# Performance work log

Measured on AMD Instinct MI355X. Metric: run time of the kernel, lower is better.

The kernel has to match this reference:

```python
import jax, jax.numpy as jnp
import numpy as np

D_MODEL = 256; N_HEADS = 8; N_LEVELS = 4; N_POINTS = 4
D_HEAD = D_MODEL // N_HEADS


def setup_inputs() -> dict:
    key = jax.random.key(0)
    ks = jax.random.split(key, 8)
    N, Lq = 4, 4096
    shapes = np.array([4096, 2048, 1024, 512], dtype=np.int32)  # temporal lengths per level
    Len_in = int(shapes.sum())  # 7680
    start = np.concatenate([[0], np.cumsum(shapes)[:-1]]).astype(np.int32)
    HLP = N_HEADS * N_LEVELS * N_POINTS
    return {
        "query": jax.random.normal(ks[0], (N, Lq, D_MODEL), jnp.float32),
        "reference_points": jax.random.uniform(ks[1], (N, Lq, N_LEVELS, 1), jnp.float32),
        "input_flatten": jax.random.normal(ks[2], (N, Len_in, D_MODEL), jnp.float32),
        "input_spatial_shapes": jnp.asarray(shapes),
        "input_level_start_index": jnp.asarray(start),
        "W_off": jax.random.normal(ks[3], (D_MODEL, HLP), jnp.float32) * 0.01,
        "b_off": jax.random.normal(ks[4], (HLP,), jnp.float32) * 2.0,
        "W_aw": jax.random.normal(ks[5], (D_MODEL, HLP), jnp.float32) * 0.02,
        "b_aw": jnp.zeros((HLP,), jnp.float32),
        "W_v": jax.random.normal(ks[6], (D_MODEL, D_MODEL), jnp.float32) / np.sqrt(D_MODEL).astype(np.float32),
        "b_v": jnp.zeros((D_MODEL,), jnp.float32),
        "W_out": jax.random.normal(ks[7], (D_MODEL, D_MODEL), jnp.float32) / np.sqrt(D_MODEL).astype(np.float32),
        "b_out": jnp.zeros((D_MODEL,), jnp.float32),
    }


def reference(query, reference_points, input_flatten, input_spatial_shapes,
              input_level_start_index, W_off, b_off, W_aw, b_aw, W_v, b_v,
              W_out, b_out):
    N, Lq, C = query.shape
    M, L, P, Dh = N_HEADS, N_LEVELS, N_POINTS, D_HEAD
    S = input_flatten.shape[1]

    value = (input_flatten @ W_v + b_v).reshape(N, S, M, Dh)
    off = (query @ W_off + b_off).reshape(N, Lq, M, L, P)
    aw = jax.nn.softmax((query @ W_aw + b_aw).reshape(N, Lq, M, L * P), axis=-1)
    aw = aw.reshape(N, Lq, M, L, P)

    # reference_points last dim == 1 branch: loc = ref + off / T_l, in [0,1]
    T = input_spatial_shapes.astype(jnp.float32)[None, None, None, :, None]  # [1,1,1,L,1]
    loc = reference_points[:, :, None, :, None, 0] + off / T  # [N,Lq,M,L,P]

    # grid_sample(align_corners=False, padding_mode='border') along W with H=1, y=0.5:
    # pixel coord x = loc*T - 0.5, clamped to [0, T-1], then linear interp.
    x = jnp.clip(loc * T - 0.5, 0.0, T - 1.0)
    x0 = jnp.floor(x)
    w1 = x - x0                                   # frac weight for right neighbor
    i0 = x0.astype(jnp.int32)
    i1 = jnp.minimum(i0 + 1, input_spatial_shapes[None, None, None, :, None] - 1)
    base = input_level_start_index[None, None, None, :, None]
    g0 = i0 + base                                # global flattened indices [N,Lq,M,L,P]
    g1 = i1 + base

    v = value.transpose(0, 2, 1, 3)               # [N,M,S,Dh]

    def gather(idx):
        idxt = idx.transpose(0, 2, 1, 3, 4).reshape(N, M, Lq * L * P, 1)
        return jnp.take_along_axis(v, idxt, axis=2).reshape(N, M, Lq, L, P, Dh)

    s0 = gather(g0)
    s1 = gather(g1)
    w1t = w1.transpose(0, 2, 1, 3, 4)[..., None]   # [N,M,Lq,L,P,1]
    samp = s0 * (1.0 - w1t) + s1 * w1t             # [N,M,Lq,L,P,Dh]

    awt = aw.transpose(0, 2, 1, 3, 4)[..., None]
    out = (samp * awt).sum(axis=(3, 4))            # [N,M,Lq,Dh]
    out = out.transpose(0, 2, 1, 3).reshape(N, Lq, M * Dh)
    return out @ W_out + b_out
```

## Files before the change

### kernel.cpp

```cpp
#include <hip/hip_runtime.h>
#include <hip/hip_bf16.h>
#include <cstddef>
#include <cstdint>

#define D_MODEL   256
#define N_HEADS   8
#define N_LEVELS  4
#define N_POINTS  4
#define D_HEAD    32
#define HLP       128
#define NBATCH    4
#define LQ        4096
#define S_LEN     7680
#define QB        8

typedef __attribute__((ext_vector_type(8))) short  short8;
typedef __attribute__((ext_vector_type(4))) float  f32x4;
typedef __attribute__((ext_vector_type(8))) unsigned short ushort8;

__device__ __forceinline__ unsigned short f2bf(float x) {
    __hip_bfloat16 h = __float2bfloat16(x);
    return *reinterpret_cast<unsigned short*>(&h);
}
__device__ __forceinline__ float bf2f(unsigned short u) {
    unsigned int v = ((unsigned int)u) << 16;
    return *reinterpret_cast<float*>(&v);
}

__device__ __forceinline__ void gload_lds16(const void* g, void* l) {
    __builtin_amdgcn_global_load_lds(
        (const __attribute__((address_space(1))) void*)g,
        (__attribute__((address_space(3))) void*)l,
        16, 0, 0);
}

__global__ __launch_bounds__(256) void prep_kernel(
    const float* __restrict__ W_v,  const float* __restrict__ W_off,
    const float* __restrict__ W_aw, const float* __restrict__ W_out,
    const float* __restrict__ b_off, const float* __restrict__ b_aw,
    unsigned short* __restrict__ Wv_t, unsigned short* __restrict__ Wcat_t,
    unsigned short* __restrict__ Wout_t, float* __restrict__ bcat)
{
    __shared__ float t[64][65];
    const int z   = blockIdx.z;
    const int k0  = blockIdx.y * 64;
    const int n0  = blockIdx.x * 64;
    const int tid = threadIdx.x;

    const float* src; int srcN; int cs; unsigned short* dst;
    if (z == 0)      { src = W_v;   srcN = 256; cs = n0;       dst = Wv_t;  }
    else if (z == 2) { src = W_out; srcN = 256; cs = n0;       dst = Wout_t;}
    else if (n0 < 128){ src = W_off; srcN = 128; cs = n0;      dst = Wcat_t;}
    else             { src = W_aw;  srcN = 128; cs = n0 - 128; dst = Wcat_t;}

    #pragma unroll
    for (int i = 0; i < 16; ++i) {
        int idx = tid + i * 256;
        int kk = idx >> 6, nn = idx & 63;
        t[kk][nn] = src[(size_t)(k0 + kk) * srcN + cs + nn];
    }
    __syncthreads();
    #pragma unroll
    for (int i = 0; i < 16; ++i) {
        int idx = tid + i * 256;
        int nn = idx >> 6, kk = idx & 63;
        dst[(size_t)(n0 + nn) * 256 + k0 + kk] = f2bf(t[kk][nn]);
    }
    if (z == 1 && blockIdx.x == 0 && blockIdx.y == 0) {
        bcat[tid] = (tid < 128) ? b_off[tid] : b_aw[tid - 128];
    }
}

__global__ __launch_bounds__(256) void gemm_vp_kernel(
    const float* __restrict__ inflat, const float* __restrict__ query,
    const unsigned short* __restrict__ Wv_t, const unsigned short* __restrict__ Wcat_t,
    const float* __restrict__ b_v, const float* __restrict__ bcat,
    unsigned short* __restrict__ value3, float* __restrict__ P)
{
    __shared__ alignas(16) unsigned short Abuf[2][4][64][8];
    __shared__ alignas(16) unsigned short Bbuf[2][8][64][8];

    const int job = blockIdx.x;
    const bool is_val = (job < 960);
    const int jj   = is_val ? job : (job - 960);
    const int row0 = (jj >> 1) * 64;
    const int col0 = (jj & 1) * 128;
    const float* A = is_val ? inflat : query;
    const unsigned short* Bt = is_val ? Wv_t : Wcat_t;
    const float* bias = is_val ? b_v : bcat;

    const int tid  = threadIdx.x;
    const int lane = tid & 63;
    const int w    = tid >> 6;
    const int lr   = lane & 15;
    const int lk   = (lane >> 4) * 8;

    const int ar = tid >> 2;
    const int ak = (tid & 3) * 8;
    const int afrag = ar >> 4;
    const int alane = ((ak >> 3) << 4) | (ar & 15);
    const float* Arow = A + (size_t)(row0 + ar) * 256 + ak;
    const unsigned short* Bcol = Bt + (size_t)(col0 + lr) * 256 + lk;

    f32x4 acc[8] = {};

    float4 pa0 = *(const float4*)(Arow);
    float4 pa1 = *(const float4*)(Arow + 4);
    #pragma unroll
    for (int c = 0; c < 2; ++c) {
        const int in = w * 2 + c;
        gload_lds16(Bcol + (size_t)in * 16 * 256, &Bbuf[0][in][0][0]);
    }

    for (int kt = 0; kt < 8; ++kt) {
        const int cur = kt & 1;
        short8 pk;
        pk[0] = (short)f2bf(pa0.x); pk[1] = (short)f2bf(pa0.y);
        pk[2] = (short)f2bf(pa0.z); pk[3] = (short)f2bf(pa0.w);
        pk[4] = (short)f2bf(pa1.x); pk[5] = (short)f2bf(pa1.y);
        pk[6] = (short)f2bf(pa1.z); pk[7] = (short)f2bf(pa1.w);
        *(short8*)&Abuf[cur][afrag][alane][0] = pk;
        __syncthreads();

        if (kt < 7) {
            const int k1 = (kt + 1) * 32;
            pa0 = *(const float4*)(Arow + k1);
            pa1 = *(const float4*)(Arow + k1 + 4);
            #pragma unroll
            for (int c = 0; c < 2; ++c) {
                const int in = w * 2 + c;
                gload_lds16(Bcol + (size_t)in * 16 * 256 + k1, &Bbuf[1 - cur][in][0][0]);
            }
        }

        const short8 af = *(const short8*)&Abuf[cur][w][lane][0];
        #pragma unroll
        for (int j = 0; j < 8; ++j) {
            const short8 bf = *(const short8*)&Bbuf[cur][j][lane][0];
            acc[j] = __builtin_amdgcn_mfma_f32_16x16x32_bf16(af, bf, acc[j], 0, 0, 0);
        }
    }

    const int prow = (lane >> 4) * 4;
    const int pcol = lane & 15;
    const int rbase = row0 + w * 16 + prow;
    if (is_val) {
        const int n  = row0 / S_LEN;
        const int s0 = row0 - n * S_LEN + w * 16 + prow;
        #pragma unroll
        for (int j = 0; j < 8; ++j) {
            const int col = col0 + j * 16 + pcol;
            const float bs = bias[col];
            const int m = col >> 5, d = col & 31;
            unsigned short* dst = value3 + ((size_t)(n * 8 + m) * S_LEN + s0) * 32 + d;
            #pragma unroll
            for (int r = 0; r < 4; ++r)
                dst[(size_t)r * 32] = f2bf(acc[j][r] + bs);
        }
    } else {
        #pragma unroll
        for (int j = 0; j < 8; ++j) {
            const int col = col0 + j * 16 + pcol;
            const float bs = bias[col];
            #pragma unroll
            for (int r = 0; r < 4; ++r)
                P[(size_t)(rbase + r) * 256 + col] = acc[j][r] + bs;
        }
    }
}

__global__ __launch_bounds__(256) void sample_kernel(
    const float* __restrict__ P, const float* __restrict__ refp,
    const int* __restrict__ shapes, const int* __restrict__ lstart,
    const unsigned short* __restrict__ value3,
    unsigned short* __restrict__ tout)
{
    __shared__ int   sG0[QB][130];
    __shared__ float sW [QB][130];
    __shared__ float sA [QB][130];
    __shared__ int   glim[4];

    const int b    = blockIdx.x;
    const int xcd  = b & 7;
    const int n    = xcd >> 1;
    const int half = xcd & 1;
    const int slot = b >> 3;
    const int q0   = (slot * 2 + half) * QB;
    const int nq0  = n * LQ + q0;
    const int tid  = threadIdx.x;

    if (tid < 4) glim[tid] = lstart[tid] + shapes[tid] - 1;

    #pragma unroll
    for (int it = 0; it < 4; ++it) {
        const int idx = tid + it * 256;
        const int q   = idx >> 7;
        const int j   = idx & 127;
        const int l   = (j >> 2) & 3;
        const int nq  = nq0 + q;
        const float off   = __builtin_nontemporal_load(P + (size_t)nq * 256 + j);
        const float logit = __builtin_nontemporal_load(P + (size_t)nq * 256 + 128 + j);
        const float ref   = __builtin_nontemporal_load(refp + (size_t)nq * N_LEVELS + l);
        const int   sh    = shapes[l];
        const float Tf    = (float)sh;
        float x = ref * Tf + off - 0.5f;
        x = fminf(fmaxf(x, 0.0f), Tf - 1.0f);
        const float x0 = floorf(x);
        sG0[q][j] = (int)x0 + lstart[l];
        sW [q][j] = x - x0;
        sA [q][j] = logit;
    }
    __syncthreads();

    const int q  = tid >> 5;
    const int r  = tid & 31;
    const int m  = r >> 2;
    const int ql = r & 3;
    const unsigned short* vb =
        value3 + (size_t)(n * 8 + m) * S_LEN * 32 + ql * 8;

    float e[16];
    float mx = -1e30f;
    #pragma unroll
    for (int i = 0; i < 16; ++i) { e[i] = sA[q][m * 16 + i]; mx = fmaxf(mx, e[i]); }
    float s = 0.f;
    #pragma unroll
    for (int i = 0; i < 16; ++i) { e[i] = __expf(e[i] - mx); s += e[i]; }
    const float rs = 1.0f / s;

    float acc[8] = {};
    #pragma unroll
    for (int i = 0; i < 16; ++i) {
        const int j = m * 16 + i;
        const float a  = e[i] * rs;
        const float ww = sW[q][j];
        const int g0 = sG0[q][j];
        const int g1 = min(g0 + 1, glim[i >> 2]);
        const ushort8 u0 = *(const ushort8*)(vb + (size_t)g0 * 32);
        const ushort8 u1 = *(const ushort8*)(vb + (size_t)g1 * 32);
        #pragma unroll
        for (int d = 0; d < 8; ++d) {
            const float v0 = bf2f(u0[d]);
            const float v1 = bf2f(u1[d]);
            acc[d] += a * (v0 + ww * (v1 - v0));
        }
    }
    ushort8 o;
    #pragma unroll
    for (int d = 0; d < 8; ++d) o[d] = f2bf(acc[d]);
    __builtin_nontemporal_store(o,
        (ushort8*)(tout + (size_t)(nq0 + q) * 256 + m * 32 + ql * 8));
}

__global__ __launch_bounds__(256) void gemm_out_kernel(
    const unsigned short* __restrict__ A,
    const unsigned short* __restrict__ Bt,
    const float* __restrict__ bias,
    float* __restrict__ Cout)
{
    __shared__ alignas(16) unsigned short Abuf[2][4][64][8];
    __shared__ alignas(16) unsigned short Bbuf[2][8][64][8];

    const int jj   = blockIdx.x;
    const int row0 = (jj >> 1) * 64;
    const int col0 = (jj & 1) * 128;

    const int tid  = threadIdx.x;
    const int lane = tid & 63;
    const int w    = tid >> 6;
    const int lr   = lane & 15;
    const int lk   = (lane >> 4) * 8;

    const unsigned short* Arow = A + (size_t)(row0 + w * 16 + lr) * 256 + lk;
    const unsigned short* Bcol = Bt + (size_t)(col0 + lr) * 256 + lk;

    f32x4 acc[8] = {};

    gload_lds16(Arow, &Abuf[0][w][0][0]);
    #pragma unroll
    for (int c = 0; c < 2; ++c) {
        const int in = w * 2 + c;
        gload_lds16(Bcol + (size_t)in * 16 * 256, &Bbuf[0][in][0][0]);
    }

    for (int kt = 0; kt < 8; ++kt) {
        const int cur = kt & 1;
        __syncthreads();

        if (kt < 7) {
            const int k1 = (kt + 1) * 32;
            gload_lds16(Arow + k1, &Abuf[1 - cur][w][0][0]);
            #pragma unroll
            for (int c = 0; c < 2; ++c) {
                const int in = w * 2 + c;
                gload_lds16(Bcol + (size_t)in * 16 * 256 + k1, &Bbuf[1 - cur][in][0][0]);
            }
        }

        const short8 af = *(const short8*)&Abuf[cur][w][lane][0];
        #pragma unroll
        for (int j = 0; j < 8; ++j) {
            const short8 bf = *(const short8*)&Bbuf[cur][j][lane][0];
            acc[j] = __builtin_amdgcn_mfma_f32_16x16x32_bf16(af, bf, acc[j], 0, 0, 0);
        }
    }

    const int prow = (lane >> 4) * 4;
    const int pcol = lane & 15;
    const int rbase = row0 + w * 16 + prow;
    #pragma unroll
    for (int j = 0; j < 8; ++j) {
        const int col = col0 + j * 16 + pcol;
        const float bs = bias[col];
        #pragma unroll
        for (int r = 0; r < 4; ++r)
            Cout[(size_t)(rbase + r) * 256 + col] = acc[j][r] + bs;
    }
}

extern "C" void kernel_launch(void* const* d_in, const int* in_sizes, int n_in,
                              void* d_out, int out_size, void* d_ws, size_t ws_size,
                              hipStream_t stream)
{
    const float* query  = (const float*)d_in[0];
    const float* refp   = (const float*)d_in[1];
    const float* inflat = (const float*)d_in[2];
    const int*   shapes = (const int*)d_in[3];
    const int*   lstart = (const int*)d_in[4];
    const float* W_off  = (const float*)d_in[5];
    const float* b_off  = (const float*)d_in[6];
    const float* W_aw   = (const float*)d_in[7];
    const float* b_aw   = (const float*)d_in[8];
    const float* W_v    = (const float*)d_in[9];
    const float* b_v    = (const float*)d_in[10];
    const float* W_out  = (const float*)d_in[11];
    const float* b_out  = (const float*)d_in[12];

    const int M_val = NBATCH * S_LEN;
    const int M_q   = NBATCH * LQ;

    char* p = (char*)d_ws;
    unsigned short* value3 = (unsigned short*)p; p += (size_t)M_val * D_MODEL * 2;
    float*          P      = (float*)p;          p += (size_t)M_q * 256 * 4;
    unsigned short* tbuf   = (unsigned short*)p; p += (size_t)M_q * D_MODEL * 2;
    unsigned short* Wv_t   = (unsigned short*)p; p += 256 * 256 * 2;
    unsigned short* Wcat_t = (unsigned short*)p; p += 256 * 256 * 2;
    unsigned short* Wout_t = (unsigned short*)p; p += 256 * 256 * 2;
    float*          bcat   = (float*)p;          p += 256 * 4;

    prep_kernel<<<dim3(4, 4, 3), 256, 0, stream>>>(
        W_v, W_off, W_aw, W_out, b_off, b_aw, Wv_t, Wcat_t, Wout_t, bcat);
    gemm_vp_kernel<<<1472, 256, 0, stream>>>(
        inflat, query, Wv_t, Wcat_t, b_v, bcat, value3, P);
    sample_kernel<<<2048, 256, 0, stream>>>(
        P, refp, shapes, lstart, value3, tbuf);
    gemm_out_kernel<<<512, 256, 0, stream>>>(
        tbuf, Wout_t, b_out, (float*)d_out);
}
```

Before: 161.7 us.

## Enlarge GEMM tiles to 2D warp layout, shrink sample blocks, batch gathers

The value/projection GEMM moves from 64-row to 128-row tiles, with a 2x2 warp layout where each warp computes a 4x4 grid of MFMA tiles. This raises fragment reuse per LDS load and halves the grid. The output GEMM switches to a 2x4 per-warp fragment layout. The sampling kernel now uses 4-query, 128-thread blocks with twice as many blocks, and issues its value gathers in batches of four before accumulating, to expose more memory-level parallelism. The costs are higher register pressure in the GEMM and fewer blocks available to hide latency in the first GEMM.

```diff
diff --git a/kernel.cpp b/kernel.cpp
--- a/kernel.cpp
+++ b/kernel.cpp
@@ -12,7 +12,7 @@
 #define NBATCH    4
 #define LQ        4096
 #define S_LEN     7680
-#define QB        8
+#define QB        4
 
 typedef __attribute__((ext_vector_type(8))) short  short8;
 typedef __attribute__((ext_vector_type(4))) float  f32x4;
@@ -77,13 +77,13 @@
     const float* __restrict__ b_v, const float* __restrict__ bcat,
     unsigned short* __restrict__ value3, float* __restrict__ P)
 {
-    __shared__ alignas(16) unsigned short Abuf[2][4][64][8];
+    __shared__ alignas(16) unsigned short Abuf[2][8][64][8];
     __shared__ alignas(16) unsigned short Bbuf[2][8][64][8];
 
     const int job = blockIdx.x;
-    const bool is_val = (job < 960);
-    const int jj   = is_val ? job : (job - 960);
-    const int row0 = (jj >> 1) * 64;
+    const bool is_val = (job < 480);
+    const int jj   = is_val ? job : (job - 480);
+    const int row0 = (jj >> 1) * 128;
     const int col0 = (jj & 1) * 128;
     const float* A = is_val ? inflat : query;
     const unsigned short* Bt = is_val ? Wv_t : Wcat_t;
@@ -92,84 +92,105 @@
     const int tid  = threadIdx.x;
     const int lane = tid & 63;
     const int w    = tid >> 6;
+    const int wm   = w & 1;
+    const int wn   = w >> 1;
     const int lr   = lane & 15;
     const int lk   = (lane >> 4) * 8;
 
-    const int ar = tid >> 2;
-    const int ak = (tid & 3) * 8;
-    const int afrag = ar >> 4;
-    const int alane = ((ak >> 3) << 4) | (ar & 15);
-    const float* Arow = A + (size_t)(row0 + ar) * 256 + ak;
+    const float* Ap0 = A + (size_t)(row0 + (w * 2 + 0) * 16 + lr) * 256 + lk;
+    const float* Ap1 = A + (size_t)(row0 + (w * 2 + 1) * 16 + lr) * 256 + lk;
     const unsigned short* Bcol = Bt + (size_t)(col0 + lr) * 256 + lk;
 
-    f32x4 acc[8] = {};
-
-    float4 pa0 = *(const float4*)(Arow);
-    float4 pa1 = *(const float4*)(Arow + 4);
+    f32x4 acc[4][4] = {};
+
+    float4 a00 = *(const float4*)(Ap0), a01 = *(const float4*)(Ap0 + 4);
+    float4 a10 = *(const float4*)(Ap1), a11 = *(const float4*)(Ap1 + 4);
     #pragma unroll
     for (int c = 0; c < 2; ++c) {
-        const int in = w * 2 + c;
-        gload_lds16(Bcol + (size_t)in * 16 * 256, &Bbuf[0][in][0][0]);
+        const int im = w * 2 + c;
+        gload_lds16(Bcol + (size_t)im * 16 * 256, &Bbuf[0][im][0][0]);
     }
 
     for (int kt = 0; kt < 8; ++kt) {
         const int cur = kt & 1;
-        short8 pk;
-        pk[0] = (short)f2bf(pa0.x); pk[1] = (short)f2bf(pa0.y);
-        pk[2] = (short)f2bf(pa0.z); pk[3] = (short)f2bf(pa0.w);
-        pk[4] = (short)f2bf(pa1.x); pk[5] = (short)f2bf(pa1.y);
-        pk[6] = (short)f2bf(pa1.z); pk[7] = (short)f2bf(pa1.w);
-        *(short8*)&Abuf[cur][afrag][alane][0] = pk;
+        {
+            short8 pk;
+            pk[0] = (short)f2bf(a00.x); pk[1] = (short)f2bf(a00.y);
+            pk[2] = (short)f2bf(a00.z); pk[3] = (short)f2bf(a00.w);
+            pk[4] = (short)f2bf(a01.x); pk[5] = (short)f2bf(a01.y);
+            pk[6] = (short)f2bf(a01.z); pk[7] = (short)f2bf(a01.w);
+            *(short8*)&Abuf[cur][w * 2 + 0][lane][0] = pk;
+            pk[0] = (short)f2bf(a10.x); pk[1] = (short)f2bf(a10.y);
+            pk[2] = (short)f2bf(a10.z); pk[3] = (short)f2bf(a10.w);
+            pk[4] = (short)f2bf(a11.x); pk[5] = (short)f2bf(a11.y);
+            pk[6] = (short)f2bf(a11.z); pk[7] = (short)f2bf(a11.w);
+            *(short8*)&Abuf[cur][w * 2 + 1][lane][0] = pk;
+        }
         __syncthreads();
 
         if (kt < 7) {
             const int k1 = (kt + 1) * 32;
-            pa0 = *(const float4*)(Arow + k1);
-            pa1 = *(const float4*)(Arow + k1 + 4);
+            a00 = *(const float4*)(Ap0 + k1); a01 = *(const float4*)(Ap0 + k1 + 4);
+            a10 = *(const float4*)(Ap1 + k1); a11 = *(const float4*)(Ap1 + k1 + 4);
             #pragma unroll
             for (int c = 0; c < 2; ++c) {
-                const int in = w * 2 + c;
-                gload_lds16(Bcol + (size_t)in * 16 * 256 + k1, &Bbuf[1 - cur][in][0][0]);
+                const int im = w * 2 + c;
+                gload_lds16(Bcol + (size_t)im * 16 * 256 + k1, &Bbuf[1 - cur][im][0][0]);
             }
         }
 
-        const short8 af = *(const short8*)&Abuf[cur][w][lane][0];
-        #pragma unroll
-        for (int j = 0; j < 8; ++j) {
-            const short8 bf = *(const short8*)&Bbuf[cur][j][lane][0];
-            acc[j] = __builtin_amdgcn_mfma_f32_16x16x32_bf16(af, bf, acc[j], 0, 0, 0);
-        }
+        short8 af[4], bfr[4];
+        #pragma unroll
+        for (int i = 0; i < 4; ++i) af[i]  = *(const short8*)&Abuf[cur][wm * 4 + i][lane][0];
+        #pragma unroll
+        for (int j = 0; j < 4; ++j) bfr[j] = *(const short8*)&Bbuf[cur][wn * 4 + j][lane][0];
+
+        #pragma unroll
+        for (int i = 0; i < 4; ++i)
+            #pragma unroll
+            for (int j = 0; j < 4; ++j)
+                acc[i][j] = __builtin_amdgcn_mfma_f32_16x16x32_bf16(
+                    af[i], bfr[j], acc[i][j], 0, 0, 0);
     }
 
     const int prow = (lane >> 4) * 4;
     const int pcol = lane & 15;
-    const int rbase = row0 + w * 16 + prow;
     if (is_val) {
         const int n  = row0 / S_LEN;
-        const int s0 = row0 - n * S_LEN + w * 16 + prow;
-        #pragma unroll
-        for (int j = 0; j < 8; ++j) {
-            const int col = col0 + j * 16 + pcol;
+        const int s0 = row0 - n * S_LEN + wm * 64;
+        #pragma unroll
+        for (int j = 0; j < 4; ++j) {
+            const int col = col0 + wn * 64 + j * 16 + pcol;
             const float bs = bias[col];
             const int m = col >> 5, d = col & 31;
             unsigned short* dst = value3 + ((size_t)(n * 8 + m) * S_LEN + s0) * 32 + d;
             #pragma unroll
-            for (int r = 0; r < 4; ++r)
-                dst[(size_t)r * 32] = f2bf(acc[j][r] + bs);
+            for (int i = 0; i < 4; ++i) {
+                #pragma unroll
+                for (int r = 0; r < 4; ++r) {
+                    const int rl = i * 16 + prow + r;
+                    dst[(size_t)rl * 32] = f2bf(acc[i][j][r] + bs);
+                }
+            }
         }
     } else {
         #pragma unroll
-        for (int j = 0; j < 8; ++j) {
-            const int col = col0 + j * 16 + pcol;
+        for (int j = 0; j < 4; ++j) {
+            const int col = col0 + wn * 64 + j * 16 + pcol;
             const float bs = bias[col];
             #pragma unroll
-            for (int r = 0; r < 4; ++r)
-                P[(size_t)(rbase + r) * 256 + col] = acc[j][r] + bs;
-        }
-    }
-}
-
-__global__ __launch_bounds__(256) void sample_kernel(
+            for (int i = 0; i < 4; ++i) {
+                #pragma unroll
+                for (int r = 0; r < 4; ++r) {
+                    const int row = row0 + wm * 64 + i * 16 + prow + r;
+                    P[(size_t)row * 256 + col] = acc[i][j][r] + bs;
+                }
+            }
+        }
+    }
+}
+
+__global__ __launch_bounds__(128) void sample_kernel(
     const float* __restrict__ P, const float* __restrict__ refp,
     const int* __restrict__ shapes, const int* __restrict__ lstart,
     const unsigned short* __restrict__ value3,
@@ -193,7 +214,7 @@
 
     #pragma unroll
     for (int it = 0; it < 4; ++it) {
-        const int idx = tid + it * 256;
+        const int idx = tid + it * 128;
         const int q   = idx >> 7;
         const int j   = idx & 127;
         const int l   = (j >> 2) & 3;
@@ -230,19 +251,28 @@
 
     float acc[8] = {};
     #pragma unroll
-    for (int i = 0; i < 16; ++i) {
-        const int j = m * 16 + i;
-        const float a  = e[i] * rs;
-        const float ww = sW[q][j];
-        const int g0 = sG0[q][j];
-        const int g1 = min(g0 + 1, glim[i >> 2]);
-        const ushort8 u0 = *(const ushort8*)(vb + (size_t)g0 * 32);
-        const ushort8 u1 = *(const ushort8*)(vb + (size_t)g1 * 32);
-        #pragma unroll
-        for (int d = 0; d < 8; ++d) {
-            const float v0 = bf2f(u0[d]);
-            const float v1 = bf2f(u1[d]);
-            acc[d] += a * (v0 + ww * (v1 - v0));
+    for (int c = 0; c < 4; ++c) {
+        ushort8 u0[4], u1[4];
+        float   aw[4], wl[4];
+        #pragma unroll
+        for (int i4 = 0; i4 < 4; ++i4) {
+            const int i = c * 4 + i4;
+            const int j = m * 16 + i;
+            aw[i4] = e[i] * rs;
+            wl[i4] = sW[q][j];
+            const int g0 = sG0[q][j];
+            const int g1 = min(g0 + 1, glim[i >> 2]);
+            u0[i4] = *(const ushort8*)(vb + (size_t)g0 * 32);
+            u1[i4] = *(const ushort8*)(vb + (size_t)g1 * 32);
+        }
+        #pragma unroll
+        for (int i4 = 0; i4 < 4; ++i4) {
+            #pragma unroll
+            for (int d = 0; d < 8; ++d) {
+                const float v0 = bf2f(u0[i4][d]);
+                const float v1 = bf2f(u1[i4][d]);
+                acc[d] += aw[i4] * (v0 + wl[i4] * (v1 - v0));
+            }
         }
     }
     ushort8 o;
@@ -268,19 +298,21 @@
     const int tid  = threadIdx.x;
     const int lane = tid & 63;
     const int w    = tid >> 6;
+    const int wm   = w & 1;
+    const int wn   = w >> 1;
     const int lr   = lane & 15;
     const int lk   = (lane >> 4) * 8;
 
     const unsigned short* Arow = A + (size_t)(row0 + w * 16 + lr) * 256 + lk;
     const unsigned short* Bcol = Bt + (size_t)(col0 + lr) * 256 + lk;
 
-    f32x4 acc[8] = {};
+    f32x4 acc[2][4] = {};
 
     gload_lds16(Arow, &Abuf[0][w][0][0]);
     #pragma unroll
     for (int c = 0; c < 2; ++c) {
-        const int in = w * 2 + c;
-        gload_lds16(Bcol + (size_t)in * 16 * 256, &Bbuf[0][in][0][0]);
+        const int im = w * 2 + c;
+        gload_lds16(Bcol + (size_t)im * 16 * 256, &Bbuf[0][im][0][0]);
     }
 
     for (int kt = 0; kt < 8; ++kt) {
@@ -292,29 +324,38 @@
             gload_lds16(Arow + k1, &Abuf[1 - cur][w][0][0]);
             #pragma unroll
             for (int c = 0; c < 2; ++c) {
-                const int in = w * 2 + c;
-                gload_lds16(Bcol + (size_t)in * 16 * 256 + k1, &Bbuf[1 - cur][in][0][0]);
+                const int im = w * 2 + c;
+                gload_lds16(Bcol + (size_t)im * 16 * 256 + k1, &Bbuf[1 - cur][im][0][0]);
             }
         }
 
-        const short8 af = *(const short8*)&Abuf[cur][w][lane][0];
-        #pragma unroll
-        for (int j = 0; j < 8; ++j) {
-            const short8 bf = *(const short8*)&Bbuf[cur][j][lane][0];
-            acc[j] = __builtin_amdgcn_mfma_f32_16x16x32_bf16(af, bf, acc[j], 0, 0, 0);
-        }
+        short8 af[2], bfr[4];
+        #pragma unroll
+        for (int i = 0; i < 2; ++i) af[i]  = *(const short8*)&Abuf[cur][wm * 2 + i][lane][0];
+        #pragma unroll
+        for (int j = 0; j < 4; ++j) bfr[j] = *(const short8*)&Bbuf[cur][wn * 4 + j][lane][0];
+
+        #pragma unroll
+        for (int i = 0; i < 2; ++i)
+            #pragma unroll
+            for (int j = 0; j < 4; ++j)
+                acc[i][j] = __builtin_amdgcn_mfma_f32_16x16x32_bf16(
+                    af[i], bfr[j], acc[i][j], 0, 0, 0);
     }
 
     const int prow = (lane >> 4) * 4;
     const int pcol = lane & 15;
-    const int rbase = row0 + w * 16 + prow;
-    #pragma unroll
-    for (int j = 0; j < 8; ++j) {
-        const int col = col0 + j * 16 + pcol;
-        const float bs = bias[col];
-        #pragma unroll
-        for (int r = 0; r < 4; ++r)
-            Cout[(size_t)(rbase + r) * 256 + col] = acc[j][r] + bs;
+    #pragma unroll
+    for (int i = 0; i < 2; ++i) {
+        #pragma unroll
+        for (int j = 0; j < 4; ++j) {
+            const int col = col0 + wn * 64 + j * 16 + pcol;
+            const float bs = bias[col];
+            const int rbase = row0 + wm * 32 + i * 16 + prow;
+            #pragma unroll
+            for (int r = 0; r < 4; ++r)
+                Cout[(size_t)(rbase + r) * 256 + col] = acc[i][j][r] + bs;
+        }
     }
 }
 
@@ -350,9 +391,9 @@
 
     prep_kernel<<<dim3(4, 4, 3), 256, 0, stream>>>(
         W_v, W_off, W_aw, W_out, b_off, b_aw, Wv_t, Wcat_t, Wout_t, bcat);
-    gemm_vp_kernel<<<1472, 256, 0, stream>>>(
+    gemm_vp_kernel<<<736, 256, 0, stream>>>(
         inflat, query, Wv_t, Wcat_t, b_v, bcat, value3, P);
-    sample_kernel<<<2048, 256, 0, stream>>>(
+    sample_kernel<<<4096, 128, 0, stream>>>(
         P, refp, shapes, lstart, value3, tbuf);
     gemm_out_kernel<<<512, 256, 0, stream>>>(
         tbuf, Wout_t, b_out, (float*)d_out);
```

Measured after the change: 168.2 us. +4.0%, slower.
